# Performance work log

Measured on AMD Instinct MI355X. Metric: run time of the kernel, lower is better.

Reference implementation:

```python
import jax, jax.numpy as jnp
import numpy as np

R_MAX, S_MAX, C_PAIR = 32, 2, 128
N_R = 2 * R_MAX + 2   # 66 buckets for residue/token distances
N_S = 2 * S_MAX + 2   # 6 buckets for chain distance


def setup_inputs() -> dict:
    key = jax.random.key(0)
    k1, k2, k3, k4 = jax.random.split(key, 4)
    B, N = 1, 1024
    residue_index = jax.random.randint(k1, (B, N), 0, 512, dtype=jnp.int32)
    token_index = jnp.broadcast_to(jnp.arange(N, dtype=jnp.int32), (B, N))
    asym_id = jnp.sort(jax.random.randint(k2, (B, N), 0, 8, dtype=jnp.int32), axis=-1)
    entity_id = jax.random.randint(k3, (B, N), 0, 4, dtype=jnp.int32)
    mask = jnp.ones((B, N), dtype=jnp.float32)
    W = jax.random.normal(k4, (C_PAIR, 2 * N_R + N_S + 1), dtype=jnp.float32) * 0.02
    return {"residue_index": residue_index, "token_index": token_index,
            "asym_id": asym_id, "entity_id": entity_id, "mask": mask, "W": W}


def _bucket(feat, cond, cmax):
    # relative_dists = feat[..., None, :] - feat[..., :, None]
    d = feat[..., None, :] - feat[..., :, None]
    return jnp.where(cond, jnp.clip(d + cmax, 0, 2 * cmax), 2 * cmax + 1)


def reference(residue_index, token_index, asym_id, entity_id, mask, W):
    same_chain = asym_id[..., :, None] == asym_id[..., None, :]
    same_res = residue_index[..., :, None] == residue_index[..., None, :]
    same_entity = entity_id[..., :, None] == entity_id[..., None, :]

    d_pos = _bucket(residue_index, same_chain, R_MAX)            # [B,N,N] in [0,65]
    d_tok = _bucket(token_index, same_chain & same_res, R_MAX)   # [B,N,N] in [0,65]
    d_chain = _bucket(asym_id, same_chain, S_MAX)                # [B,N,N] in [0,5]

    # one_hot(d) @ W.T == gather rows of W.T per bucket, then sum the blocks:
    # concat layout along input_dim: [rel_pos(66) | rel_token(66) | same_entity(1) | rel_chain(6)]
    Wt = W.T                              # [139, c_pair]
    W_pos = Wt[:N_R]                      # [66, c]
    W_tok = Wt[N_R:2 * N_R]               # [66, c]
    W_ent = Wt[2 * N_R]                   # [c]
    W_chain = Wt[2 * N_R + 1:]            # [6, c]

    p_ij = (W_pos[d_pos] + W_tok[d_tok]
            + same_entity[..., None].astype(W.dtype) * W_ent
            + W_chain[d_chain])           # [B,N,N,c_pair]

    pair_mask = (mask[..., :, None] * mask[..., None, :])[..., None]
    return p_ij * pair_mask
```

## Files before the change

kernel.cpp:

```cpp
#include <hip/hip_runtime.h>


#define N_TOK 1024
#define C_PAIR 128
#define NR 66
#define NS 6
#define W_COLS 139
#define ROWS 140

__global__ __launch_bounds__(1024, 8)
void relpos_kernel(const int* __restrict__ ri, const int* __restrict__ ti,
                   const int* __restrict__ ai, const int* __restrict__ ei,
                   const float* __restrict__ mask, const float* __restrict__ W,
                   float* __restrict__ out, int nblocks_stride) {
    __shared__ float wt[ROWS * C_PAIR];

    for (int idx = threadIdx.x; idx < ROWS * C_PAIR; idx += blockDim.x) {
        int k = idx >> 7;
        int c = idx & 127;
        wt[idx] = (k < W_COLS) ? W[c * W_COLS + k] : 0.0f;
    }
    __syncthreads();

    const int total = N_TOK * N_TOK * (C_PAIR / 4);
    const int stride = nblocks_stride;
    float4* __restrict__ out4 = (float4*)out;

    for (int g = blockIdx.x * blockDim.x + threadIdx.x; g < total; g += stride) {
        int c4   = g & 31;
        int pair = g >> 5;
        int j = pair & (N_TOK - 1);
        int i = pair >> 10;

        int   r_i = ri[i], r_j = ri[j];
        int   t_i = ti[i], t_j = ti[j];
        int   a_i = ai[i], a_j = ai[j];
        int   e_i = ei[i], e_j = ei[j];
        float m   = mask[i] * mask[j];

        bool same_chain = (a_i == a_j);
        bool same_res   = (r_i == r_j);
        bool same_ent   = (e_i == e_j);

        int dp = same_chain              ? min(max(r_j - r_i + 32, 0), 64) : 65;
        int dt = (same_chain && same_res)? min(max(t_j - t_i + 32, 0), 64) : 65;
        int dc = same_chain              ? min(max(a_j - a_i + 2,  0), 4)  : 5;
        int re = same_ent ? (2 * NR) : (ROWS - 1);

        const float4* wp = (const float4*)&wt[dp * C_PAIR];
        const float4* wk = (const float4*)&wt[(NR + dt) * C_PAIR];
        const float4* we = (const float4*)&wt[re * C_PAIR];
        const float4* wc = (const float4*)&wt[(2 * NR + 1 + dc) * C_PAIR];

        float4 a = wp[c4];
        float4 b = wk[c4];
        float4 e = we[c4];
        float4 c = wc[c4];

        float4 v;
        v.x = (a.x + b.x + e.x + c.x) * m;
        v.y = (a.y + b.y + e.y + c.y) * m;
        v.z = (a.z + b.z + e.z + c.z) * m;
        v.w = (a.w + b.w + e.w + c.w) * m;

        out4[g] = v;
    }
}

extern "C" void kernel_launch(void* const* d_in, const int* in_sizes, int n_in,
                              void* d_out, int out_size, void* d_ws, size_t ws_size,
                              hipStream_t stream) {
    const int*   ri   = (const int*)d_in[0];
    const int*   ti   = (const int*)d_in[1];
    const int*   ai   = (const int*)d_in[2];
    const int*   ei   = (const int*)d_in[3];
    const float* mask = (const float*)d_in[4];
    const float* W    = (const float*)d_in[5];
    float*       out  = (float*)d_out;

    const int threads = 1024;
    const int blocks  = 512;
    relpos_kernel<<<blocks, threads, 0, stream>>>(ri, ti, ai, ei, mask, W, out,
                                                  blocks * threads);
}
```

Before: 121.3 us.

## Process four channel chunks per thread with nontemporal stores and coalesced W load

Each thread now handles one pair with 8-lane stride over four float4 chunks, so the per-pair index loads and bucket math are amortized over 16 channels instead of 4. Output writes use nontemporal stores to bypass cache pollution for the 512MB streaming write. The W staging loop now reads global memory contiguously and transposes into shared memory. The trade-off is fewer in-flight threads per pair and a strided store pattern within a wave.

```diff
diff --git a/kernel.cpp b/kernel.cpp
--- a/kernel.cpp
+++ b/kernel.cpp
@@ -8,27 +8,31 @@
 #define W_COLS 139
 #define ROWS 140
 
+typedef float f32x4 __attribute__((ext_vector_type(4)));
+
 __global__ __launch_bounds__(1024, 8)
 void relpos_kernel(const int* __restrict__ ri, const int* __restrict__ ti,
                    const int* __restrict__ ai, const int* __restrict__ ei,
                    const float* __restrict__ mask, const float* __restrict__ W,
-                   float* __restrict__ out, int nblocks_stride) {
+                   float* __restrict__ out) {
     __shared__ float wt[ROWS * C_PAIR];
 
-    for (int idx = threadIdx.x; idx < ROWS * C_PAIR; idx += blockDim.x) {
-        int k = idx >> 7;
-        int c = idx & 127;
-        wt[idx] = (k < W_COLS) ? W[c * W_COLS + k] : 0.0f;
+    for (int idx = threadIdx.x; idx < C_PAIR * W_COLS; idx += blockDim.x) {
+        int c = idx / W_COLS;
+        int k = idx - c * W_COLS;
+        wt[k * C_PAIR + c] = W[idx];
     }
+    for (int idx = threadIdx.x; idx < C_PAIR; idx += blockDim.x)
+        wt[(ROWS - 1) * C_PAIR + idx] = 0.0f;
     __syncthreads();
 
-    const int total = N_TOK * N_TOK * (C_PAIR / 4);
-    const int stride = nblocks_stride;
-    float4* __restrict__ out4 = (float4*)out;
+    const int total  = N_TOK * N_TOK * 8;
+    const int stride = gridDim.x * blockDim.x;
+    f32x4* __restrict__ out4 = (f32x4*)out;
 
-    for (int g = blockIdx.x * blockDim.x + threadIdx.x; g < total; g += stride) {
-        int c4   = g & 31;
-        int pair = g >> 5;
+    for (int t = blockIdx.x * blockDim.x + threadIdx.x; t < total; t += stride) {
+        int c4   = t & 7;
+        int pair = t >> 3;
         int j = pair & (N_TOK - 1);
         int i = pair >> 10;
 
@@ -40,30 +44,24 @@
 
         bool same_chain = (a_i == a_j);
         bool same_res   = (r_i == r_j);
-        bool same_ent   = (e_i == e_j);
 
-        int dp = same_chain              ? min(max(r_j - r_i + 32, 0), 64) : 65;
-        int dt = (same_chain && same_res)? min(max(t_j - t_i + 32, 0), 64) : 65;
-        int dc = same_chain              ? min(max(a_j - a_i + 2,  0), 4)  : 5;
-        int re = same_ent ? (2 * NR) : (ROWS - 1);
+        int dp = same_chain               ? min(max(r_j - r_i + 32, 0), 64) : 65;
+        int dt = (same_chain && same_res) ? min(max(t_j - t_i + 32, 0), 64) : 65;
+        int dc = same_chain               ? min(max(a_j - a_i + 2,  0), 4)  : 5;
+        int re = (e_i == e_j) ? (2 * NR) : (ROWS - 1);
 
-        const float4* wp = (const float4*)&wt[dp * C_PAIR];
-        const float4* wk = (const float4*)&wt[(NR + dt) * C_PAIR];
-        const float4* we = (const float4*)&wt[re * C_PAIR];
-        const float4* wc = (const float4*)&wt[(2 * NR + 1 + dc) * C_PAIR];
+        const f32x4* wp = (const f32x4*)&wt[dp * C_PAIR];
+        const f32x4* wk = (const f32x4*)&wt[(NR + dt) * C_PAIR];
+        const f32x4* we = (const f32x4*)&wt[re * C_PAIR];
+        const f32x4* wc = (const f32x4*)&wt[(2 * NR + 1 + dc) * C_PAIR];
 
-        float4 a = wp[c4];
-        float4 b = wk[c4];
-        float4 e = we[c4];
-        float4 c = wc[c4];
-
-        float4 v;
-        v.x = (a.x + b.x + e.x + c.x) * m;
-        v.y = (a.y + b.y + e.y + c.y) * m;
-        v.z = (a.z + b.z + e.z + c.z) * m;
-        v.w = (a.w + b.w + e.w + c.w) * m;
-
-        out4[g] = v;
+        int base = pair * 32 + c4;
+        #pragma unroll
+        for (int q = 0; q < 4; ++q) {
+            int cc = c4 + 8 * q;
+            f32x4 v = (wp[cc] + wk[cc] + we[cc] + wc[cc]) * m;
+            __builtin_nontemporal_store(v, &out4[base + 8 * q]);
+        }
     }
 }
 
@@ -80,6 +78,5 @@
 
     const int threads = 1024;
     const int blocks  = 512;
-    relpos_kernel<<<blocks, threads, 0, stream>>>(ri, ti, ai, ei, mask, W, out,
-                                                  blocks * threads);
+    relpos_kernel<<<blocks, threads, 0, stream>>>(ri, ti, ai, ei, mask, W, out);
 }
```

Result: faster. 115.1 us (median of 2 runs) (-5.1%).
